# Optimization experiments

Hardware: AMD Instinct MI355X
Metric: run time of the kernel (lower is better)

Reference implementation:

```python
import jax, jax.numpy as jnp
import numpy as np

B = 4
N_PER_B = 65536
N = B * N_PER_B
GROUP_SIZE = 64
ORDER = 9  # min bits to cover grid size 512
C0, C1, C2 = 64, 128, 128


def hilbert_encode(coors, order):
    """Skilling AxesToTranspose, vectorized over N points, 3 dims -> int32 code."""
    n = 3
    X = [coors[:, i].astype(jnp.int32) for i in range(n)]
    M = 1 << (order - 1)
    Q = M
    while Q > 1:
        P = Q - 1
        for i in range(n):
            cond = (X[i] & Q) != 0
            if i == 0:
                X[0] = jnp.where(cond, X[0] ^ P, X[0])
            else:
                t = (X[0] ^ X[i]) & P
                x0 = jnp.where(cond, X[0] ^ P, X[0] ^ t)
                xi = jnp.where(cond, X[i], X[i] ^ t)
                X[0], X[i] = x0, xi
        Q >>= 1
    for i in range(1, n):
        X[i] = X[i] ^ X[i - 1]
    t = jnp.zeros_like(X[0])
    Q = M
    while Q > 1:
        t = jnp.where((X[n - 1] & Q) != 0, t ^ (Q - 1), t)
        Q >>= 1
    X = [x ^ t for x in X]
    # interleave transposed bits MSB-first: code has 3*order bits (27 < 31, fits int32)
    code = jnp.zeros_like(X[0])
    for b in range(order - 1, -1, -1):
        for i in range(n):
            code = (code << 1) | ((X[i] >> b) & 1)
    return code


def _mapping_indices(vox_coors):
    """Two Hilbert orderings (normal + reversed coord axes); per-batch stable grouping."""
    batch = vox_coors[:, 0]
    c1 = vox_coors[:, 1:4]
    c2 = vox_coors[:, 3:0:-1]  # [0,3,2,1] reverse of the xyz columns
    code1 = hilbert_encode(c1, ORDER)
    code2 = hilbert_encode(c2, ORDER)
    ind1 = jnp.lexsort((code1, batch))  # batch-major, curve-order minor
    ind2 = jnp.lexsort((code2, batch))
    inv1 = jnp.argsort(ind1)
    ind12 = inv1[ind2]  # maps ordering-1 arrangement to ordering-2 arrangement
    return ind1, ind12


def _block(p, x, params):
    """VoxFormer-style block: center pts per group, pos-encode, gate feats, local attn, FFN."""
    Wpos, bpos, Wq, Wk, Wv, Wo, Wout = params
    C = Wq.shape[0]
    gs = GROUP_SIZE
    pg = p.reshape(-1, gs, 3)
    e = (pg - pg.mean(axis=1, keepdims=True)).reshape(-1, 3) @ Wpos + bpos  # [N,C]
    h = (x * e).reshape(-1, gs, C)  # [G,gs,C]
    q, k, v = h @ Wq, h @ Wk, h @ Wv
    scores = jnp.einsum('gqc,gkc->gqk', q, k) / jnp.sqrt(jnp.asarray(C, q.dtype))
    attn = jax.nn.softmax(scores, axis=-1)
    o = jnp.einsum('gqk,gkc->gqc', attn, v).reshape(-1, C) @ Wo
    return jax.nn.relu(o) @ Wout  # [N,C_out]


def setup_inputs() -> dict:
    key = jax.random.key(0)
    ks = jax.random.split(key, 20)
    bcol = jnp.repeat(jnp.arange(B, dtype=jnp.int32), N_PER_B)
    z = jax.random.randint(ks[0], (N,), 0, 64, dtype=jnp.int32)
    y = jax.random.randint(ks[1], (N,), 0, 512, dtype=jnp.int32)
    x = jax.random.randint(ks[2], (N,), 0, 512, dtype=jnp.int32)
    vox_coors = jnp.stack([bcol, z, y, x], axis=1)
    vox_numbs = jnp.full((B,), N_PER_B, dtype=jnp.int32)
    vox_feats = jax.random.normal(ks[3], (N, C0), dtype=jnp.float32)
    pts_coors = jax.random.normal(ks[4], (N, 3), dtype=jnp.float32)
    s = lambda k, shape: jax.random.normal(k, shape, dtype=jnp.float32) / np.float32(np.sqrt(shape[0]))
    return dict(
        vox_numbs=vox_numbs, vox_coors=vox_coors, vox_feats=vox_feats, pts_coors=pts_coors,
        Wpos1=s(ks[5], (3, C0)), bpos1=jnp.zeros((C0,), jnp.float32),
        Wq1=s(ks[6], (C0, C0)), Wk1=s(ks[7], (C0, C0)), Wv1=s(ks[8], (C0, C0)),
        Wo1=s(ks[9], (C0, C0)), Wout1=s(ks[10], (C0, C1)),
        Wpos2=s(ks[11], (3, C1)), bpos2=jnp.zeros((C1,), jnp.float32),
        Wq2=s(ks[12], (C1, C1)), Wk2=s(ks[13], (C1, C1)), Wv2=s(ks[14], (C1, C1)),
        Wo2=s(ks[15], (C1, C1)), Wout2=s(ks[16], (C1, C2)),
    )


def reference(vox_numbs, vox_coors, vox_feats, pts_coors,
              Wpos1, bpos1, Wq1, Wk1, Wv1, Wo1, Wout1,
              Wpos2, bpos2, Wq2, Wk2, Wv2, Wo2, Wout2):
    ind1, ind12 = _mapping_indices(vox_coors)
    params = ((Wpos1, bpos1, Wq1, Wk1, Wv1, Wo1, Wout1),
              (Wpos2, bpos2, Wq2, Wk2, Wv2, Wo2, Wout2))
    for ind, prm in zip((ind1, ind12), params):
        vox_feats = vox_feats[ind]
        pts_coors = pts_coors[ind]
        vox_coors = vox_coors[ind]
        vox_feats = _block(pts_coors, vox_feats, prm)
    return vox_feats, pts_coors, vox_coors, vox_numbs
```

## Files before the change

### kernel.cpp

```cpp
#include <hip/hip_runtime.h>

using u64 = unsigned long long;
typedef _Float16 f16;
using f16x8 = __attribute__((ext_vector_type(8))) _Float16;
using f16x4 = __attribute__((ext_vector_type(4))) _Float16;
using f32x4 = __attribute__((ext_vector_type(4))) float;

__device__ __forceinline__ int hilbert3(int X0, int X1, int X2) {
  #pragma unroll
  for (int Q = 256; Q > 1; Q >>= 1) {
    const int P = Q - 1;
    if (X0 & Q) X0 ^= P;
    int t1 = (X0 ^ X1) & P;
    if (X1 & Q) X0 ^= P; else { X0 ^= t1; X1 ^= t1; }
    int t2 = (X0 ^ X2) & P;
    if (X2 & Q) X0 ^= P; else { X0 ^= t2; X2 ^= t2; }
  }
  X1 ^= X0;
  X2 ^= X1;
  int t = 0;
  #pragma unroll
  for (int Q = 256; Q > 1; Q >>= 1) if (X2 & Q) t ^= (Q - 1);
  X0 ^= t; X1 ^= t; X2 ^= t;
  int code = 0;
  #pragma unroll
  for (int b = 8; b >= 0; b--)
    code = (code << 3) | (((X0 >> b) & 1) << 2) | (((X1 >> b) & 1) << 1) | ((X2 >> b) & 1);
  return code;
}

__device__ __forceinline__ void cswap(u64& a, u64& b, bool up) {
  if ((a > b) == up) { u64 t = a; a = b; b = t; }
}

__global__ __launch_bounds__(1024) void sort_tile0(const int* __restrict__ vox,
                                                   u64* __restrict__ keys, int n,
                                                   int spanm1) {
  __shared__ u64 s[4096];
  const int base = blockIdx.x * 4096;
  const int bl = base & spanm1;
  #pragma unroll
  for (int m = 0; m < 4; m++) {
    const int e = base + threadIdx.x + m * 1024;
    const int isrc = e & (n - 1);
    const int4 c = ((const int4*)vox)[isrc];
    const unsigned code = (e < n) ? (unsigned)hilbert3(c.y, c.z, c.w)
                                  : (unsigned)hilbert3(c.w, c.z, c.y);
    s[threadIdx.x + m * 1024] =
        ((u64)(unsigned)c.x << 45) | ((u64)code << 18) | (unsigned)isrc;
  }
  __syncthreads();
  for (int k = 2; k <= 4096; k <<= 1) {
    for (int j = k >> 1; j >= 1; j >>= 1) {
      #pragma unroll
      for (int m = 0; m < 2; m++) {
        const int p = threadIdx.x + m * 1024;
        const int i = ((p & ~(j - 1)) << 1) | (p & (j - 1));
        const bool up = (((bl + i) & k) == 0);
        u64 a = s[i], b = s[i | j];
        if ((a > b) == up) { s[i] = b; s[i | j] = a; }
      }
      __syncthreads();
    }
  }
  #pragma unroll
  for (int m = 0; m < 4; m++)
    keys[base + threadIdx.x + m * 1024] = s[threadIdx.x + m * 1024];
}

template<int LEV>
__device__ __forceinline__ void gstepT(u64* __restrict__ keys, int t, int jlow,
                                       int k, int spanm1) {
  constexpr int S = 1 << LEV;
  const int i0 = ((t & ~(jlow - 1)) << LEV) | (t & (jlow - 1));
  const bool up = (((i0 & spanm1) & k) == 0);
  u64 x[S];
  #pragma unroll
  for (int m = 0; m < S; m++) x[m] = keys[i0 + (size_t)m * jlow];
  #pragma unroll
  for (int d = S >> 1; d >= 1; d >>= 1)
    #pragma unroll
    for (int m = 0; m < S; m++)
      if (!(m & d)) cswap(x[m], x[m | d], up);
  #pragma unroll
  for (int m = 0; m < S; m++) keys[i0 + (size_t)m * jlow] = x[m];
}

__global__ void bitonic_gN(u64* __restrict__ keys, int jlow, int lev, int k, int spanm1) {
  const int t = blockIdx.x * blockDim.x + threadIdx.x;
  switch (lev) {
    case 1: gstepT<1>(keys, t, jlow, k, spanm1); break;
    case 2: gstepT<2>(keys, t, jlow, k, spanm1); break;
    case 3: gstepT<3>(keys, t, jlow, k, spanm1); break;
    default: gstepT<4>(keys, t, jlow, k, spanm1); break;
  }
}

__global__ __launch_bounds__(1024) void merge_tile4(u64* __restrict__ keys, int k,
                                                    int spanm1) {
  __shared__ u64 s[4096];
  const int base = blockIdx.x * 4096;
  #pragma unroll
  for (int m = 0; m < 4; m++)
    s[threadIdx.x + m * 1024] = keys[base + threadIdx.x + m * 1024];
  __syncthreads();
  const bool up = (((base & spanm1) & k) == 0);
  for (int j = 2048; j >= 1; j >>= 1) {
    #pragma unroll
    for (int m = 0; m < 2; m++) {
      const int p = threadIdx.x + m * 1024;
      const int i = ((p & ~(j - 1)) << 1) | (p & (j - 1));
      u64 a = s[i], b = s[i | j];
      if ((a > b) == up) { s[i] = b; s[i | j] = a; }
    }
    __syncthreads();
  }
  #pragma unroll
  for (int m = 0; m < 4; m++)
    keys[base + threadIdx.x + m * 1024] = s[threadIdx.x + m * 1024];
}

__global__ void extract_inv_k(const u64* __restrict__ keys, const float* __restrict__ pts,
                              int* __restrict__ ind, int* __restrict__ inv,
                              float* __restrict__ pts1p, int n) {
  int t = blockIdx.x * blockDim.x + threadIdx.x;
  if (t >= n) return;
  int s = (int)(keys[t] & 0x3FFFFULL);
  ind[t] = s;
  inv[s] = t;
  pts1p[t * 3 + 0] = pts[s * 3 + 0];
  pts1p[t * 3 + 1] = pts[s * 3 + 1];
  pts1p[t * 3 + 2] = pts[s * 3 + 2];
}

__global__ void finish_k(const u64* __restrict__ keys2, const int* __restrict__ inv1,
                         int* __restrict__ g2, const float* __restrict__ pts,
                         const int* __restrict__ vox, const int* __restrict__ numbs,
                         float* __restrict__ out_pts, float* __restrict__ out_vox,
                         float* __restrict__ out_nb, int n, int B) {
  int t = blockIdx.x * blockDim.x + threadIdx.x;
  if (t >= n) return;
  int s = (int)(keys2[t] & 0x3FFFFULL);
  g2[t] = inv1[s];
  out_pts[t * 3 + 0] = pts[s * 3 + 0];
  out_pts[t * 3 + 1] = pts[s * 3 + 1];
  out_pts[t * 3 + 2] = pts[s * 3 + 2];
  const int4 v = ((const int4*)vox)[s];
  out_vox[t * 4 + 0] = (float)v.x;
  out_vox[t * 4 + 1] = (float)v.y;
  out_vox[t * 4 + 2] = (float)v.z;
  out_vox[t * 4 + 3] = (float)v.w;
  if (t < B) out_nb[t] = (float)numbs[t];
}

__global__ void prep_all(const float* __restrict__ Wq1, const float* __restrict__ Wk1,
                         const float* __restrict__ Wv1, const float* __restrict__ Wo1,
                         const float* __restrict__ Wout1,
                         const float* __restrict__ Wq2, const float* __restrict__ Wk2,
                         const float* __restrict__ Wv2, const float* __restrict__ Wo2,
                         const float* __restrict__ Wout2,
                         f16* __restrict__ A1a, f16* __restrict__ A2a, f16* __restrict__ A3a,
                         f16* __restrict__ A1b, f16* __restrict__ A2b, f16* __restrict__ A3b) {
  const int idx = blockIdx.x * blockDim.x + threadIdx.x;
  if (idx < 4096) {
    const int a = idx >> 6, b = idx & 63;
    float s1 = 0.f, s2 = 0.f;
    for (int c = 0; c < 64; c++) {
      s1 = fmaf(Wq1[b * 64 + c], Wk1[a * 64 + c], s1);
      s2 = fmaf(Wv1[b * 64 + c], Wo1[c * 64 + a], s2);
    }
    A1a[idx] = (f16)(s1 * 0.125f);
    A2a[idx] = (f16)s2;
  }
  if (idx < 8192) {
    const int o = idx >> 6, c = idx & 63;
    A3a[idx] = (f16)Wout1[c * 128 + o];
  }
  {
    const int a = idx >> 7, b = idx & 127;
    float s1 = 0.f, s2 = 0.f;
    for (int c = 0; c < 128; c++) {
      s1 = fmaf(Wq2[b * 128 + c], Wk2[a * 128 + c], s1);
      s2 = fmaf(Wv2[b * 128 + c], Wo2[c * 128 + a], s2);
    }
    A1b[idx] = (f16)(s1 * 0.08838834764831845f);
    A2b[idx] = (f16)s2;
    A3b[idx] = (f16)Wout2[b * 128 + a];
  }
}

__device__ __forceinline__ int swzb(int row) { return ((row ^ (row >> 3)) & 7) << 4; }

template<int M, int K, int AMODE>
__device__ __forceinline__ void gemmT(const f16* __restrict__ Ag, const f16* __restrict__ lA,
                                      const f16* __restrict__ lB, int w, int lane,
                                      f32x4 (&acc)[M / 64][4]) {
  constexpr int CT = M / 64;
  const int lr = lane & 15, lk = lane >> 4;
  #pragma unroll
  for (int ks = 0; ks < K / 32; ks++) {
    const int k0 = ks * 32 + lk * 8;
    f16x8 Af[CT];
    #pragma unroll
    for (int ct = 0; ct < CT; ct++) {
      const int c = lr + (w * CT + ct) * 16;
      if (AMODE == 0) {
        Af[ct] = *(const f16x8*)(Ag + (size_t)c * K + k0);
      } else if (AMODE == 1) {
        Af[ct] = *(const f16x8*)((const char*)lA + (((c * K + k0) * 2) ^ swzb(c)));
      } else {
        f16x8 a;
        #pragma unroll
        for (int e = 0; e < 8; e++) {
          const int j = k0 + e;
          a[e] = *(const f16*)((const char*)lA + (((j * M + c) * 2) ^ swzb(j)));
        }
        Af[ct] = a;
      }
    }
    f16x8 Bf[4];
    #pragma unroll
    for (int qt = 0; qt < 4; qt++) {
      const int q = lr + qt * 16;
      Bf[qt] = *(const f16x8*)((const char*)lB + (((q * K + k0) * 2) ^ swzb(q)));
    }
    #pragma unroll
    for (int ct = 0; ct < CT; ct++)
      #pragma unroll
      for (int qt = 0; qt < 4; qt++)
        acc[ct][qt] = __builtin_amdgcn_mfma_f32_16x16x32_f16(Af[ct], Bf[qt], acc[ct][qt], 0, 0, 0);
  }
}

template<int M, bool RELU>
__device__ __forceinline__ void storeT16(f16* __restrict__ dst, int w, int lane,
                                         const f32x4 (&acc)[M / 64][4]) {
  constexpr int CT = M / 64;
  #pragma unroll
  for (int ct = 0; ct < CT; ct++)
    #pragma unroll
    for (int qt = 0; qt < 4; qt++) {
      const int q = (lane & 15) + qt * 16;
      const int c0 = (w * CT + ct) * 16 + (lane >> 4) * 4;
      f16x4 v;
      #pragma unroll
      for (int r = 0; r < 4; r++) {
        float x = acc[ct][qt][r];
        if (RELU) x = fmaxf(x, 0.f);
        v[r] = (f16)x;
      }
      *(f16x4*)((char*)dst + (((q * M + c0) * 2) ^ swzb(q))) = v;
    }
}

template<int C, bool X16, bool OUT16>
__global__ __launch_bounds__(512, 4) void block_mfma(
    const int* __restrict__ idx_x, const float* __restrict__ ptsP,
    const void* __restrict__ xsrc,
    const float* __restrict__ Wpos, const float* __restrict__ bpos,
    const f16* __restrict__ A1, const f16* __restrict__ A2, const f16* __restrict__ A3,
    void* __restrict__ outp) {
  constexpr int CT = C / 64;
  constexpr int GSZ = 64 * C * 4 + 8192;
  extern __shared__ char smem_raw[];
  char* smem = smem_raw + (threadIdx.x >> 8) * GSZ;
  f16* bufH = (f16*)smem;
  f16* bufT = bufH + 64 * C;
  f16* scH  = bufT + 64 * C;

  const int g = blockIdx.x * 2 + (threadIdx.x >> 8);
  const int t = threadIdx.x & 255;
  const int lane = t & 63;
  const int w = t >> 6;
  const int lr = lane & 15, lk = lane >> 4;

  f16x8 A1f[C / 32][CT];
  #pragma unroll
  for (int ks = 0; ks < C / 32; ks++)
    #pragma unroll
    for (int ct = 0; ct < CT; ct++)
      A1f[ks][ct] = *(const f16x8*)(A1 + (size_t)(lr + (w * CT + ct) * 16) * C + ks * 32 + lk * 8);

  const int q = t >> 2, qq = t & 3;
  const int sx = idx_x[g * 64 + q];
  float xv[C / 4];
  if (X16) {
    #pragma unroll
    for (int i = 0; i < C / 32; i++) {
      f16x8 xr = *(const f16x8*)((const f16*)xsrc + (size_t)sx * C + qq * (C / 4) + i * 8);
      #pragma unroll
      for (int j = 0; j < 8; j++) xv[i * 8 + j] = (float)xr[j];
    }
  } else {
    #pragma unroll
    for (int i = 0; i < C / 16; i++) {
      float4 x0 = *(const float4*)((const float*)xsrc + (size_t)sx * C + qq * (C / 4) + i * 4);
      xv[i * 4 + 0] = x0.x; xv[i * 4 + 1] = x0.y; xv[i * 4 + 2] = x0.z; xv[i * 4 + 3] = x0.w;
    }
  }

  {
    float mx = ptsP[(g * 64 + lane) * 3 + 0];
    float my = ptsP[(g * 64 + lane) * 3 + 1];
    float mz = ptsP[(g * 64 + lane) * 3 + 2];
    #pragma unroll
    for (int o = 32; o > 0; o >>= 1) {
      mx += __shfl_xor(mx, o); my += __shfl_xor(my, o); mz += __shfl_xor(mz, o);
    }
    mx *= (1.f / 64.f); my *= (1.f / 64.f); mz *= (1.f / 64.f);

    const float d0 = ptsP[(g * 64 + q) * 3 + 0] - mx;
    const float d1 = ptsP[(g * 64 + q) * 3 + 1] - my;
    const float d2 = ptsP[(g * 64 + q) * 3 + 2] - mz;
    #pragma unroll
    for (int i = 0; i < C / 32; i++) {
      const int c0 = qq * (C / 4) + i * 8;
      f16x8 hv;
      #pragma unroll
      for (int jj = 0; jj < 8; jj += 4) {
        const float4 w0 = *(const float4*)(Wpos + 0 * C + c0 + jj);
        const float4 w1 = *(const float4*)(Wpos + 1 * C + c0 + jj);
        const float4 w2 = *(const float4*)(Wpos + 2 * C + c0 + jj);
        const float4 bb = *(const float4*)(bpos + c0 + jj);
        hv[jj + 0] = (f16)(xv[i * 8 + jj + 0] * fmaf(d0, w0.x, fmaf(d1, w1.x, fmaf(d2, w2.x, bb.x))));
        hv[jj + 1] = (f16)(xv[i * 8 + jj + 1] * fmaf(d0, w0.y, fmaf(d1, w1.y, fmaf(d2, w2.y, bb.y))));
        hv[jj + 2] = (f16)(xv[i * 8 + jj + 2] * fmaf(d0, w0.z, fmaf(d1, w1.z, fmaf(d2, w2.z, bb.z))));
        hv[jj + 3] = (f16)(xv[i * 8 + jj + 3] * fmaf(d0, w0.w, fmaf(d1, w1.w, fmaf(d2, w2.w, bb.w))));
      }
      *(f16x8*)((char*)bufH + (((q * C + c0) * 2) ^ swzb(q))) = hv;
    }
  }
  __syncthreads();

  {
    f32x4 acc[CT][4] = {};
    #pragma unroll
    for (int ks = 0; ks < C / 32; ks++) {
      const int k0 = ks * 32 + lk * 8;
      f16x8 Bf[4];
      #pragma unroll
      for (int qt = 0; qt < 4; qt++) {
        const int qr = lr + qt * 16;
        Bf[qt] = *(const f16x8*)((const char*)bufH + (((qr * C + k0) * 2) ^ swzb(qr)));
      }
      #pragma unroll
      for (int ct = 0; ct < CT; ct++)
        #pragma unroll
        for (int qt = 0; qt < 4; qt++)
          acc[ct][qt] = __builtin_amdgcn_mfma_f32_16x16x32_f16(A1f[ks][ct], Bf[qt], acc[ct][qt], 0, 0, 0);
    }
    storeT16<C, false>(bufT, w, lane, acc);
  }
  __syncthreads();

  {
    f32x4 acc[1][4] = {};
    gemmT<64, C, 1>(nullptr, bufH, bufT, w, lane, acc);
    #pragma unroll
    for (int qt = 0; qt < 4; qt++) {
      const int qr = lr + qt * 16;
      const int j0 = w * 16 + lk * 4;
      f16x4 v;
      #pragma unroll
      for (int r = 0; r < 4; r++) v[r] = (f16)acc[0][qt][r];
      *(f16x4*)((char*)scH + (((qr * 64 + j0) * 2) ^ swzb(qr))) = v;
    }
  }
  __syncthreads();

  {
    float v[16];
    float mxv = -3.0e38f;
    #pragma unroll
    for (int i = 0; i < 2; i++) {
      f16x8 x8 = *(const f16x8*)((const char*)scH + (((q * 64 + qq * 16 + i * 8) * 2) ^ swzb(q)));
      #pragma unroll
      for (int j = 0; j < 8; j++) {
        v[i * 8 + j] = (float)x8[j];
        mxv = fmaxf(mxv, v[i * 8 + j]);
      }
    }
    mxv = fmaxf(mxv, __shfl_xor(mxv, 1));
    mxv = fmaxf(mxv, __shfl_xor(mxv, 2));
    float s = 0.f;
    #pragma unroll
    for (int i = 0; i < 16; i++) { v[i] = __expf(v[i] - mxv); s += v[i]; }
    s += __shfl_xor(s, 1);
    s += __shfl_xor(s, 2);
    const float inv = 1.f / s;
    #pragma unroll
    for (int i = 0; i < 2; i++) {
      f16x8 pk;
      #pragma unroll
      for (int j = 0; j < 8; j++) pk[j] = (f16)(v[i * 8 + j] * inv);
      *(f16x8*)((char*)scH + (((q * 64 + qq * 16 + i * 8) * 2) ^ swzb(q))) = pk;
    }
  }
  __syncthreads();

  {
    f32x4 acc[CT][4] = {};
    gemmT<C, 64, 2>(nullptr, bufH, scH, w, lane, acc);
    storeT16<C, false>(bufT, w, lane, acc);
  }
  __syncthreads();

  {
    f32x4 acc[CT][4] = {};
    gemmT<C, C, 0>(A2, nullptr, bufT, w, lane, acc);
    storeT16<C, true>(bufH, w, lane, acc);
  }
  __syncthreads();

  {
    f32x4 acc[2][4] = {};
    gemmT<128, C, 0>(A3, nullptr, bufH, w, lane, acc);
    #pragma unroll
    for (int ct = 0; ct < 2; ct++)
      #pragma unroll
      for (int qt = 0; qt < 4; qt++) {
        const int qr = (lane & 15) + qt * 16;
        const int o0 = (w * 2 + ct) * 16 + (lane >> 4) * 4;
        const size_t row = (size_t)g * 64 + qr;
        if (OUT16) {
          f16x4 v;
          #pragma unroll
          for (int r = 0; r < 4; r++) v[r] = (f16)acc[ct][qt][r];
          *(f16x4*)((f16*)outp + row * 128 + o0) = v;
        } else {
          *(f32x4*)((float*)outp + row * 128 + o0) = acc[ct][qt];
        }
      }
  }
}

extern "C" void kernel_launch(void* const* d_in, const int* in_sizes, int n_in,
                              void* d_out, int out_size, void* d_ws, size_t ws_size,
                              hipStream_t stream) {
  const int*   vox_numbs = (const int*)d_in[0];
  const int*   vox_coors = (const int*)d_in[1];
  const float* vox_feats = (const float*)d_in[2];
  const float* pts_coors = (const float*)d_in[3];
  const float* Wpos1 = (const float*)d_in[4];
  const float* bpos1 = (const float*)d_in[5];
  const float* Wq1   = (const float*)d_in[6];
  const float* Wk1   = (const float*)d_in[7];
  const float* Wv1   = (const float*)d_in[8];
  const float* Wo1   = (const float*)d_in[9];
  const float* Wout1 = (const float*)d_in[10];
  const float* Wpos2 = (const float*)d_in[11];
  const float* bpos2 = (const float*)d_in[12];
  const float* Wq2   = (const float*)d_in[13];
  const float* Wk2   = (const float*)d_in[14];
  const float* Wv2   = (const float*)d_in[15];
  const float* Wo2   = (const float*)d_in[16];
  const float* Wout2 = (const float*)d_in[17];

  const int B = in_sizes[0];
  const int n = in_sizes[1] / 4;
  const int ngrp = n / 64;

  char* w = (char*)d_ws;
  auto alloc = [&](size_t bytes) {
    char* p = w;
    w += (bytes + 255) & ~(size_t)255;
    return p;
  };
  u64* keys    = (u64*)alloc((size_t)2 * n * 8);
  int* ind1    = (int*)alloc((size_t)n * 4);
  int* inv1    = (int*)alloc((size_t)n * 4);
  int* g2      = (int*)alloc((size_t)n * 4);
  float* pts1p = (float*)alloc((size_t)n * 3 * 4);
  f16* A1a     = (f16*)alloc(64 * 64 * 2);
  f16* A2a     = (f16*)alloc(64 * 64 * 2);
  f16* A3a     = (f16*)alloc(128 * 64 * 2);
  f16* A1b     = (f16*)alloc(128 * 128 * 2);
  f16* A2b     = (f16*)alloc(128 * 128 * 2);
  f16* A3b     = (f16*)alloc(128 * 128 * 2);
  f16* feats1  = (f16*)alloc((size_t)n * 128 * 2);
  u64* keys2   = keys + n;

  float* out_feats = (float*)d_out;
  float* out_pts   = out_feats + (size_t)n * 128;
  float* out_vox   = out_pts + (size_t)n * 3;
  float* out_nb    = out_vox + (size_t)n * 4;

  auto f64k  = block_mfma<64,  false, true>;
  auto f128k = block_mfma<128, true,  false>;
  hipFuncSetAttribute((const void*)f64k,  hipFuncAttributeMaxDynamicSharedMemorySize, 65536);
  hipFuncSetAttribute((const void*)f128k, hipFuncAttributeMaxDynamicSharedMemorySize, 98304);

  prep_all<<<64, 256, 0, stream>>>(Wq1, Wk1, Wv1, Wo1, Wout1, Wq2, Wk2, Wv2, Wo2, Wout2,
                                   A1a, A2a, A3a, A1b, A2b, A3b);

  int span = (B > 0) ? n / B : n;
  if (span < 8192 || (span & (span - 1)) != 0 || n % span != 0) span = n;
  const int spanm1 = span - 1;

  sort_tile0<<<2 * n / 4096, 1024, 0, stream>>>(vox_coors, keys, n, spanm1);
  for (int k = 8192; k <= span; k <<= 1) {
    int j = k >> 1;
    while (j >= 4096) {
      int lev = 1;
      while (lev < 4 && (j >> lev) >= 4096) lev++;
      const int jlow = j >> (lev - 1);
      const int nth = (2 * n) >> lev;
      bitonic_gN<<<nth / 256, 256, 0, stream>>>(keys, jlow, lev, k, spanm1);
      j = jlow >> 1;
    }
    merge_tile4<<<2 * n / 4096, 1024, 0, stream>>>(keys, k, spanm1);
  }

  extract_inv_k<<<(n + 255) / 256, 256, 0, stream>>>(keys, pts_coors, ind1, inv1, pts1p, n);
  finish_k<<<(n + 255) / 256, 256, 0, stream>>>(keys2, inv1, g2, pts_coors, vox_coors,
                                                vox_numbs, out_pts, out_vox, out_nb, n, B);

  block_mfma<64, false, true><<<ngrp / 2, 512, 2 * 24576, stream>>>(
      ind1, pts1p, vox_feats, Wpos1, bpos1, A1a, A2a, A3a, feats1);
  block_mfma<128, true, false><<<ngrp / 2, 512, 2 * 40960, stream>>>(
      g2, out_pts, feats1, Wpos2, bpos2, A1b, A2b, A3b, out_feats);
}
```

Baseline: 305.9 us.

## Use 8192-key sort tiles, one group per block, and new LDS swizzle

The shared-memory bitonic sort and merge tiles are templated and raised from 4096 to 8192 keys (64 KB LDS), which removes one global bitonic pass level per merge stage. The attention kernels now process one 64-point group per 256-thread block instead of two groups per 512-thread block, which changes LDS per block and scheduling granularity. The LDS swizzle function is also changed to a different XOR pattern. Larger sort tiles reduce occupancy of the sort kernels, and the smaller attention blocks mean more blocks to launch and schedule.

```diff
diff --git a/kernel.cpp b/kernel.cpp
--- a/kernel.cpp
+++ b/kernel.cpp
@@ -33,14 +33,15 @@
   if ((a > b) == up) { u64 t = a; a = b; b = t; }
 }
 
+template<int TILE>
 __global__ __launch_bounds__(1024) void sort_tile0(const int* __restrict__ vox,
                                                    u64* __restrict__ keys, int n,
                                                    int spanm1) {
-  __shared__ u64 s[4096];
-  const int base = blockIdx.x * 4096;
+  __shared__ u64 s[TILE];
+  const int base = blockIdx.x * TILE;
   const int bl = base & spanm1;
   #pragma unroll
-  for (int m = 0; m < 4; m++) {
+  for (int m = 0; m < TILE / 1024; m++) {
     const int e = base + threadIdx.x + m * 1024;
     const int isrc = e & (n - 1);
     const int4 c = ((const int4*)vox)[isrc];
@@ -50,10 +51,10 @@
         ((u64)(unsigned)c.x << 45) | ((u64)code << 18) | (unsigned)isrc;
   }
   __syncthreads();
-  for (int k = 2; k <= 4096; k <<= 1) {
+  for (int k = 2; k <= TILE; k <<= 1) {
     for (int j = k >> 1; j >= 1; j >>= 1) {
       #pragma unroll
-      for (int m = 0; m < 2; m++) {
+      for (int m = 0; m < TILE / 2048; m++) {
         const int p = threadIdx.x + m * 1024;
         const int i = ((p & ~(j - 1)) << 1) | (p & (j - 1));
         const bool up = (((bl + i) & k) == 0);
@@ -64,7 +65,7 @@
     }
   }
   #pragma unroll
-  for (int m = 0; m < 4; m++)
+  for (int m = 0; m < TILE / 1024; m++)
     keys[base + threadIdx.x + m * 1024] = s[threadIdx.x + m * 1024];
 }
 
@@ -96,18 +97,19 @@
   }
 }
 
-__global__ __launch_bounds__(1024) void merge_tile4(u64* __restrict__ keys, int k,
-                                                    int spanm1) {
-  __shared__ u64 s[4096];
-  const int base = blockIdx.x * 4096;
-  #pragma unroll
-  for (int m = 0; m < 4; m++)
+template<int TILE>
+__global__ __launch_bounds__(1024) void merge_tile(u64* __restrict__ keys, int k,
+                                                   int spanm1) {
+  __shared__ u64 s[TILE];
+  const int base = blockIdx.x * TILE;
+  #pragma unroll
+  for (int m = 0; m < TILE / 1024; m++)
     s[threadIdx.x + m * 1024] = keys[base + threadIdx.x + m * 1024];
   __syncthreads();
   const bool up = (((base & spanm1) & k) == 0);
-  for (int j = 2048; j >= 1; j >>= 1) {
-    #pragma unroll
-    for (int m = 0; m < 2; m++) {
+  for (int j = TILE / 2; j >= 1; j >>= 1) {
+    #pragma unroll
+    for (int m = 0; m < TILE / 2048; m++) {
       const int p = threadIdx.x + m * 1024;
       const int i = ((p & ~(j - 1)) << 1) | (p & (j - 1));
       u64 a = s[i], b = s[i | j];
@@ -116,7 +118,7 @@
     __syncthreads();
   }
   #pragma unroll
-  for (int m = 0; m < 4; m++)
+  for (int m = 0; m < TILE / 1024; m++)
     keys[base + threadIdx.x + m * 1024] = s[threadIdx.x + m * 1024];
 }
 
@@ -189,7 +191,9 @@
   }
 }
 
-__device__ __forceinline__ int swzb(int row) { return ((row ^ (row >> 3)) & 7) << 4; }
+__device__ __forceinline__ int swzb(int row) {
+  return (((row & 7) ^ (((row >> 3) & 3) << 1)) << 4);
+}
 
 template<int M, int K, int AMODE>
 __device__ __forceinline__ void gemmT(const f16* __restrict__ Ag, const f16* __restrict__ lA,
@@ -254,22 +258,20 @@
 }
 
 template<int C, bool X16, bool OUT16>
-__global__ __launch_bounds__(512, 4) void block_mfma(
+__global__ __launch_bounds__(256, 4) void block_mfma(
     const int* __restrict__ idx_x, const float* __restrict__ ptsP,
     const void* __restrict__ xsrc,
     const float* __restrict__ Wpos, const float* __restrict__ bpos,
     const f16* __restrict__ A1, const f16* __restrict__ A2, const f16* __restrict__ A3,
     void* __restrict__ outp) {
   constexpr int CT = C / 64;
-  constexpr int GSZ = 64 * C * 4 + 8192;
-  extern __shared__ char smem_raw[];
-  char* smem = smem_raw + (threadIdx.x >> 8) * GSZ;
+  extern __shared__ char smem[];
   f16* bufH = (f16*)smem;
   f16* bufT = bufH + 64 * C;
   f16* scH  = bufT + 64 * C;
 
-  const int g = blockIdx.x * 2 + (threadIdx.x >> 8);
-  const int t = threadIdx.x & 255;
+  const int g = blockIdx.x;
+  const int t = threadIdx.x;
   const int lane = t & 63;
   const int w = t >> 6;
   const int lr = lane & 15, lk = lane >> 4;
@@ -488,35 +490,43 @@
   auto f64k  = block_mfma<64,  false, true>;
   auto f128k = block_mfma<128, true,  false>;
   hipFuncSetAttribute((const void*)f64k,  hipFuncAttributeMaxDynamicSharedMemorySize, 65536);
-  hipFuncSetAttribute((const void*)f128k, hipFuncAttributeMaxDynamicSharedMemorySize, 98304);
+  hipFuncSetAttribute((const void*)f128k, hipFuncAttributeMaxDynamicSharedMemorySize, 65536);
 
   prep_all<<<64, 256, 0, stream>>>(Wq1, Wk1, Wv1, Wo1, Wout1, Wq2, Wk2, Wv2, Wo2, Wout2,
                                    A1a, A2a, A3a, A1b, A2b, A3b);
 
   int span = (B > 0) ? n / B : n;
-  if (span < 8192 || (span & (span - 1)) != 0 || n % span != 0) span = n;
+  if (span < 4096 || (span & (span - 1)) != 0 || n % span != 0) span = n;
   const int spanm1 = span - 1;
-
-  sort_tile0<<<2 * n / 4096, 1024, 0, stream>>>(vox_coors, keys, n, spanm1);
-  for (int k = 8192; k <= span; k <<= 1) {
+  const int TILE = ((n % 8192) == 0 && span >= 8192) ? 8192 : 4096;
+
+  if (TILE == 8192)
+    sort_tile0<8192><<<2 * n / 8192, 1024, 0, stream>>>(vox_coors, keys, n, spanm1);
+  else
+    sort_tile0<4096><<<2 * n / 4096, 1024, 0, stream>>>(vox_coors, keys, n, spanm1);
+
+  for (int k = 2 * TILE; k <= span; k <<= 1) {
     int j = k >> 1;
-    while (j >= 4096) {
+    while (j >= TILE) {
       int lev = 1;
-      while (lev < 4 && (j >> lev) >= 4096) lev++;
+      while (lev < 4 && (j >> lev) >= TILE) lev++;
       const int jlow = j >> (lev - 1);
       const int nth = (2 * n) >> lev;
       bitonic_gN<<<nth / 256, 256, 0, stream>>>(keys, jlow, lev, k, spanm1);
       j = jlow >> 1;
     }
-    merge_tile4<<<2 * n / 4096, 1024, 0, stream>>>(keys, k, spanm1);
+    if (TILE == 8192)
+      merge_tile<8192><<<2 * n / 8192, 1024, 0, stream>>>(keys, k, spanm1);
+    else
+      merge_tile<4096><<<2 * n / 4096, 1024, 0, stream>>>(keys, k, spanm1);
   }
 
   extract_inv_k<<<(n + 255) / 256, 256, 0, stream>>>(keys, pts_coors, ind1, inv1, pts1p, n);
   finish_k<<<(n + 255) / 256, 256, 0, stream>>>(keys2, inv1, g2, pts_coors, vox_coors,
                                                 vox_numbs, out_pts, out_vox, out_nb, n, B);
 
-  block_mfma<64, false, true><<<ngrp / 2, 512, 2 * 24576, stream>>>(
+  block_mfma<64, false, true><<<ngrp, 256, 24576, stream>>>(
       ind1, pts1p, vox_feats, Wpos1, bpos1, A1a, A2a, A3a, feats1);
-  block_mfma<128, true, false><<<ngrp / 2, 512, 2 * 40960, stream>>>(
+  block_mfma<128, true, false><<<ngrp, 256, 40960, stream>>>(
       g2, out_pts, feats1, Wpos2, bpos2, A1b, A2b, A3b, out_feats);
 }
```

Measured after the change: 342.1 us. 11.8% more time.
